# Kernel optimization log

Hardware: AMD Instinct MI355X
Metric: run time of the kernel (lower is better)

The kernel has to match this reference:

```python
import jax, jax.numpy as jnp
import numpy as np

MAX_ITER = 10
EPSILON = 1e-4


def setup_inputs() -> dict:
    key = jax.random.key(0)
    k1, k2 = jax.random.split(key)
    B, N1, N2 = 128, 512, 512
    s = jax.random.uniform(k1, (B, N1, N2), dtype=jnp.float32)
    # per-sample effective sizes; original module assumes nrows[b] == ncols[b]
    nrows = jax.random.randint(k2, (B,), 256, N1 + 1, dtype=jnp.int32)
    ncols = nrows
    return {"s": s, "nrows": nrows, "ncols": ncols}


def reference(s, nrows, ncols):
    """Faithful BiStochastic (masked Sinkhorn) forward.

    Even iter i: column-normalize within the [ncols, ncols] top-left block,
    zero everything outside the block (matches s * tmp with tmp zero outside).
    Odd  iter i: row-normalize within the [nrows, nrows] block, zero outside.
    """
    B, n1, n2 = s.shape
    i1 = jnp.arange(n1)
    i2 = jnp.arange(n2)
    # masks derived from the block-ones matrices in the original code
    cmask_r = i1[None, :] < ncols[:, None]           # [B, n1] rows < ncols
    cmask_c = i2[None, :] < ncols[:, None]           # [B, n2] cols < ncols
    rmask_r = i1[None, :] < nrows[:, None]           # [B, n1] rows < nrows
    rmask_c = i2[None, :] < nrows[:, None]           # [B, n2] cols < nrows
    col_block = cmask_r[:, :, None] & cmask_c[:, None, :]  # [B, n1, n2]
    row_block = rmask_r[:, :, None] & rmask_c[:, None, :]  # [B, n1, n2]

    s = s + EPSILON
    for i in range(MAX_ITER):
        if i % 2 == 0:
            # col_sum[b, c] = sum_{r < ncols[b]} s[b, r, c]
            col_sum = jnp.sum(jnp.where(cmask_r[:, :, None], s, 0.0),
                              axis=1, keepdims=True)          # [B, 1, n2]
            denom = jnp.where(col_block, col_sum, 1.0)
            s = jnp.where(col_block, s, 0.0) / denom
        else:
            # row_sum[b, r] = sum_{c < nrows[b]} s[b, r, c]
            row_sum = jnp.sum(jnp.where(rmask_c[:, None, :], s, 0.0),
                              axis=2, keepdims=True)          # [B, n1, 1]
            denom = jnp.where(row_block, row_sum, 1.0)
            s = jnp.where(row_block, s, 0.0) / denom
    return s
```

## Files before the change

### kernel.cpp

```cpp
#include <hip/hip_runtime.h>

#define N     512
#define NSP   4
#define SC    128
#define EPS   1e-4f

#define MROW  65
#define LDS_U   (512 * MROW + 512 + 128 * 33 + 128 + 64)
#define LDS_BYTES (LDS_U * 4)

union U32H { unsigned int u; _Float16 h[2]; };
__device__ inline float h_lo(unsigned int x){ U32H t; t.u = x; return (float)t.h[0]; }
__device__ inline float h_hi(unsigned int x){ U32H t; t.u = x; return (float)t.h[1]; }
__device__ inline unsigned int h_pk(float a, float b){ U32H t; t.h[0]=(_Float16)a; t.h[1]=(_Float16)b; return t.u; }

typedef _Float16 half2v __attribute__((ext_vector_type(2)));
#if __has_builtin(__builtin_amdgcn_fdot2)
__device__ inline float dot2(unsigned int m, unsigned int v, float c){
    return __builtin_amdgcn_fdot2(__builtin_bit_cast(half2v, m), __builtin_bit_cast(half2v, v), c, false);
}
#else
__device__ inline float dot2(unsigned int m, unsigned int v, float c){
    return c + h_lo(m)*h_lo(v) + h_hi(m)*h_hi(v);
}
#endif

typedef unsigned int uint4v __attribute__((ext_vector_type(4)));

__device__ inline void rp_store(float* p, float v){
    __hip_atomic_store(p, v, __ATOMIC_RELAXED, __HIP_MEMORY_SCOPE_AGENT);
}
__device__ inline float rp_load(float* p){
    return __hip_atomic_load(p, __ATOMIC_RELAXED, __HIP_MEMORY_SCOPE_AGENT);
}


#define SAMPLE_SYNC() do {                                                    \
    asm volatile("s_waitcnt vmcnt(0)" ::: "memory");                          \
    __syncthreads();                                                          \
    ++phase;                                                                  \
    if (t == 0) {                                                             \
        __hip_atomic_fetch_add(barb, 1u, __ATOMIC_RELAXED,                    \
                               __HIP_MEMORY_SCOPE_AGENT);                     \
        const unsigned int tgt_ = (unsigned int)(phase * NSP);                \
        while (__hip_atomic_fetch_add(barb, 0u, __ATOMIC_RELAXED,             \
                                      __HIP_MEMORY_SCOPE_AGENT) < tgt_) {     \
            __builtin_amdgcn_s_sleep(8);                                      \
        }                                                                     \
    }                                                                         \
    __syncthreads();                                                          \
} while (0)

#define COL_REDUCE() do {                                                     \
    _Pragma("unroll")                                                         \
    for (int k_ = 0; k_ < 8; ++k_) sh[(8*j + k_)*33 + part] = acc[k_];        \
    __syncthreads();                                                          \
    if (t < 128) {                                                            \
        float s_ = 0.f;                                                       \
        _Pragma("unroll")                                                     \
        for (int p_ = 0; p_ < 32; ++p_) s_ += sh[t*33 + p_];                  \
        vf[t] = (c0 + t < n) ? 1.f / s_ : 0.f;                                \
    }                                                                         \
    __syncthreads();                                                          \
    if (t < 64) vpk[t] = h_pk(vf[2*t], vf[2*t+1]);                            \
    __syncthreads();                                                          \
} while (0)

#define ROW_PART(RPOUT) do {                                                  \
    const unsigned int vp0_ = vpk[4*j+0], vp1_ = vpk[4*j+1];                  \
    const unsigned int vp2_ = vpk[4*j+2], vp3_ = vpk[4*j+3];                  \
    _Pragma("unroll")                                                         \
    for (int it_ = 0; it_ < 16; ++it_) {                                      \
        float p_ = dot2(m[it_][0], vp0_, 0.f);                                \
        p_ = dot2(m[it_][1], vp1_, p_);                                       \
        p_ = dot2(m[it_][2], vp2_, p_);                                       \
        p_ = dot2(m[it_][3], vp3_, p_);                                       \
        sh[(it_*32 + part)*17 + j] = p_;                                      \
    }                                                                         \
    __syncthreads();                                                          \
    {                                                                         \
        float s_ = 0.f;                                                       \
        _Pragma("unroll")                                                     \
        for (int q_ = 0; q_ < 16; ++q_) s_ += sh[t*17 + q_];                  \
        rp_store((RPOUT) + rpOff + t, s_);                                    \
    }                                                                         \
    __syncthreads();                                                          \
} while (0)

__global__ __launch_bounds__(512, 2)
void k_fused(const float* __restrict__ A, const int* __restrict__ nrows,
             float* __restrict__ rpA, float* __restrict__ rpB,
             float* __restrict__ out, unsigned int* __restrict__ bar) {
    __shared__ float sh[512*17];
    __shared__ float uu[512];
    __shared__ float vf[128];
    __shared__ unsigned int vpk[64];

    const int b = blockIdx.y, sp = blockIdx.x, c0 = sp * SC;
    const int n = nrows[b];
    const int t = threadIdx.x;
    const int l = t & 63;
    const int j = l & 15;
    const int part = (t >> 6) * 4 + (l >> 4);
    const size_t baseA = (size_t)b * N * N;
    const int cb = c0 + 8*j;
    const size_t rpOff = ((size_t)b * NSP + sp) * N;
    const size_t rpB0  = (size_t)b * NSP * N;
    unsigned int* barb = bar + (size_t)b * 32;
    int phase = 0;

    uint4v m[16];
    float acc[8];

    {
        bool cok0 = (cb+0) < n, cok1 = (cb+1) < n, cok2 = (cb+2) < n, cok3 = (cb+3) < n;
        bool cok4 = (cb+4) < n, cok5 = (cb+5) < n, cok6 = (cb+6) < n, cok7 = (cb+7) < n;
#pragma unroll
        for (int k = 0; k < 8; ++k) acc[k] = 0.f;
#pragma unroll
        for (int it = 0; it < 16; ++it) {
            const int r = it*32 + part;
            const float4* p = (const float4*)(A + baseA + (size_t)r*N + cb);
            float4 a0 = p[0], a1 = p[1];
            const bool rok = r < n;
            float e0 = (rok & cok0) ? a0.x + EPS : 0.f;
            float e1 = (rok & cok1) ? a0.y + EPS : 0.f;
            float e2 = (rok & cok2) ? a0.z + EPS : 0.f;
            float e3 = (rok & cok3) ? a0.w + EPS : 0.f;
            float e4 = (rok & cok4) ? a1.x + EPS : 0.f;
            float e5 = (rok & cok5) ? a1.y + EPS : 0.f;
            float e6 = (rok & cok6) ? a1.z + EPS : 0.f;
            float e7 = (rok & cok7) ? a1.w + EPS : 0.f;
            acc[0] += e0; acc[1] += e1; acc[2] += e2; acc[3] += e3;
            acc[4] += e4; acc[5] += e5; acc[6] += e6; acc[7] += e7;
            m[it][0] = h_pk(e0, e1);
            m[it][1] = h_pk(e2, e3);
            m[it][2] = h_pk(e4, e5);
            m[it][3] = h_pk(e6, e7);
        }
    }
    COL_REDUCE();
    ROW_PART(rpA);
    SAMPLE_SYNC();

    float* rIn = rpA; float* rOut = rpB;
    for (int ps = 0; ps < 4; ++ps) {
        {
            float s = rp_load(rIn + rpB0 + 0*N + t) + rp_load(rIn + rpB0 + 1*N + t)
                    + rp_load(rIn + rpB0 + 2*N + t) + rp_load(rIn + rpB0 + 3*N + t);
            uu[t] = (t < n) ? 1.f / s : 0.f;
        }
        __syncthreads();
#pragma unroll
        for (int k = 0; k < 8; ++k) acc[k] = 0.f;
#pragma unroll
        for (int it = 0; it < 16; ++it) {
            const float ur = uu[it*32 + part];
            acc[0] += ur * h_lo(m[it][0]);
            acc[1] += ur * h_hi(m[it][0]);
            acc[2] += ur * h_lo(m[it][1]);
            acc[3] += ur * h_hi(m[it][1]);
            acc[4] += ur * h_lo(m[it][2]);
            acc[5] += ur * h_hi(m[it][2]);
            acc[6] += ur * h_lo(m[it][3]);
            acc[7] += ur * h_hi(m[it][3]);
        }
        COL_REDUCE();
        ROW_PART(rOut);
        SAMPLE_SYNC();
        float* tmp = rIn; rIn = rOut; rOut = tmp;
    }

    {
        float s = rp_load(rIn + rpB0 + 0*N + t) + rp_load(rIn + rpB0 + 1*N + t)
                + rp_load(rIn + rpB0 + 2*N + t) + rp_load(rIn + rpB0 + 3*N + t);
        uu[t] = (t < n) ? 1.f / s : 0.f;
    }
    __syncthreads();
    const float v0 = vf[8*j+0], v1 = vf[8*j+1], v2 = vf[8*j+2], v3 = vf[8*j+3];
    const float v4 = vf[8*j+4], v5 = vf[8*j+5], v6 = vf[8*j+6], v7 = vf[8*j+7];
#pragma unroll
    for (int it = 0; it < 16; ++it) {
        const int r = it*32 + part;
        const float ur = uu[r];
        float4 o0, o1;
        o0.x = h_lo(m[it][0]) * ur * v0;
        o0.y = h_hi(m[it][0]) * ur * v1;
        o0.z = h_lo(m[it][1]) * ur * v2;
        o0.w = h_hi(m[it][1]) * ur * v3;
        o1.x = h_lo(m[it][2]) * ur * v4;
        o1.y = h_hi(m[it][2]) * ur * v5;
        o1.z = h_lo(m[it][3]) * ur * v6;
        o1.w = h_hi(m[it][3]) * ur * v7;
        float4* q = (float4*)(out + baseA + (size_t)r*N + cb);
        q[0] = o0; q[1] = o1;
    }
}


__device__ inline void pass_tail(unsigned int* M2, float* red, float* vf, unsigned int* vpk,
                                 const float acc[8], int t, int part, int j, int c0, int n,
                                 int b, int sp, float* __restrict__ rp_out,
                                 float* __restrict__ vf_out) {
#pragma unroll
    for (int k = 0; k < 8; ++k) red[(8*j + k)*33 + part] = acc[k];
    __syncthreads();
    if (t < 128) {
        float s = 0.f;
#pragma unroll
        for (int p = 0; p < 32; ++p) s += red[t*33 + p];
        float v = (c0 + t < n) ? 1.f / s : 0.f;
        vf[t] = v;
        if (vf_out) vf_out[b*N + c0 + t] = v;
    }
    __syncthreads();
    if (t < 64) vpk[t] = h_pk(vf[2*t], vf[2*t+1]);
    __syncthreads();
    float p = 0.f;
    const unsigned int* row = M2 + t * MROW;
#pragma unroll
    for (int q = 0; q < 64; ++q) p = dot2(row[q], vpk[q], p);
    rp_out[((size_t)b*NSP + sp)*N + t] = p;
}

__global__ __launch_bounds__(512)
void k_pass0(const float* __restrict__ A, const int* __restrict__ nrows,
             unsigned int* __restrict__ Abf, float* __restrict__ rp_out) {
    extern __shared__ unsigned int lds[];
    unsigned int* M2 = lds;
    float* uu = (float*)(lds + 512*MROW);
    float* red = uu + 512;
    float* vf  = red + 128*33;
    unsigned int* vpk = (unsigned int*)(vf + 128);

    const int b = blockIdx.y, sp = blockIdx.x, c0 = sp * SC;
    const int n = nrows[b];
    const int t = threadIdx.x;
    const int w = t >> 6, l = t & 63;
    const int j = l & 15, rg = l >> 4;
    const size_t baseA = (size_t)b * N * N;
    const size_t baseH = (size_t)b * N * (N/2);
    const int cb = c0 + 8*j;

    bool cok[8];
#pragma unroll
    for (int k = 0; k < 8; ++k) cok[k] = (cb + k) < n;

    float acc[8] = {0,0,0,0,0,0,0,0};
    for (int it = 0; it < 16; ++it) {
        int r = it*32 + w*4 + rg;
        const float4* p = (const float4*)(A + baseA + (size_t)r*N + cb);
        float4 a0 = p[0], a1 = p[1];
        bool rok = r < n;
        float e[8];
        e[0] = (rok && cok[0]) ? a0.x + EPS : 0.f;
        e[1] = (rok && cok[1]) ? a0.y + EPS : 0.f;
        e[2] = (rok && cok[2]) ? a0.z + EPS : 0.f;
        e[3] = (rok && cok[3]) ? a0.w + EPS : 0.f;
        e[4] = (rok && cok[4]) ? a1.x + EPS : 0.f;
        e[5] = (rok && cok[5]) ? a1.y + EPS : 0.f;
        e[6] = (rok && cok[6]) ? a1.z + EPS : 0.f;
        e[7] = (rok && cok[7]) ? a1.w + EPS : 0.f;
#pragma unroll
        for (int k = 0; k < 8; ++k) acc[k] += e[k];
        uint4 q;
        q.x = h_pk(e[0], e[1]); q.y = h_pk(e[2], e[3]);
        q.z = h_pk(e[4], e[5]); q.w = h_pk(e[6], e[7]);
        *(uint4*)(Abf + baseH + (size_t)r*(N/2) + c0/2 + 4*j) = q;
        unsigned int* dst = M2 + r*MROW + 4*j;
        dst[0] = q.x; dst[1] = q.y; dst[2] = q.z; dst[3] = q.w;
    }
    (void)uu;
    pass_tail(M2, red, vf, vpk, acc, t, w*4 + rg, j, c0, n, b, sp, rp_out, nullptr);
}

__global__ __launch_bounds__(512)
void k_passN(const unsigned int* __restrict__ Abf, const int* __restrict__ nrows,
             const float* __restrict__ rp_in, float* __restrict__ rp_out,
             float* __restrict__ vf_out) {
    extern __shared__ unsigned int lds[];
    unsigned int* M2 = lds;
    float* uu = (float*)(lds + 512*MROW);
    float* red = uu + 512;
    float* vf  = red + 128*33;
    unsigned int* vpk = (unsigned int*)(vf + 128);

    const int b = blockIdx.y, sp = blockIdx.x, c0 = sp * SC;
    const int n = nrows[b];
    const int t = threadIdx.x;
    const int w = t >> 6, l = t & 63;
    const int j = l & 15, rg = l >> 4;
    const size_t baseH = (size_t)b * N * (N/2);

    {
        float s = rp_in[((size_t)b*NSP + 0)*N + t]
                + rp_in[((size_t)b*NSP + 1)*N + t]
                + rp_in[((size_t)b*NSP + 2)*N + t]
                + rp_in[((size_t)b*NSP + 3)*N + t];
        uu[t] = (t < n) ? 1.f / s : 0.f;
    }
    __syncthreads();

    float acc[8] = {0,0,0,0,0,0,0,0};
    for (int it = 0; it < 16; ++it) {
        int r = it*32 + w*4 + rg;
        uint4 q = *(const uint4*)(Abf + baseH + (size_t)r*(N/2) + c0/2 + 4*j);
        float ur = uu[r];
        acc[0] += ur * h_lo(q.x); acc[1] += ur * h_hi(q.x);
        acc[2] += ur * h_lo(q.y); acc[3] += ur * h_hi(q.y);
        acc[4] += ur * h_lo(q.z); acc[5] += ur * h_hi(q.z);
        acc[6] += ur * h_lo(q.w); acc[7] += ur * h_hi(q.w);
        unsigned int* dst = M2 + r*MROW + 4*j;
        dst[0] = q.x; dst[1] = q.y; dst[2] = q.z; dst[3] = q.w;
    }
    __syncthreads();
    pass_tail(M2, red, vf, vpk, acc, t, w*4 + rg, j, c0, n, b, sp, rp_out, vf_out);
}

__global__ __launch_bounds__(512)
void k_epi(const float* __restrict__ A, const int* __restrict__ nrows,
           const float* __restrict__ rp9, const float* __restrict__ vf8,
           float* __restrict__ out) {
    const int b = blockIdx.y;
    const int n = nrows[b];
    const int t = threadIdx.x;
    const int r = blockIdx.x*4 + (t >> 7);
    const int c = (t & 127) * 4;
    float s = rp9[((size_t)b*NSP + 0)*N + r]
            + rp9[((size_t)b*NSP + 1)*N + r]
            + rp9[((size_t)b*NSP + 2)*N + r]
            + rp9[((size_t)b*NSP + 3)*N + r];
    float ur = (r < n) ? 1.f / s : 0.f;
    float4 v = *(const float4*)(vf8 + b*N + c);
    const size_t off = (size_t)b*N*N + (size_t)r*N + c;
    float4 a = *(const float4*)(A + off);
    float4 o;
    o.x = (a.x + EPS) * ur * v.x;
    o.y = (a.y + EPS) * ur * v.y;
    o.z = (a.z + EPS) * ur * v.z;
    o.w = (a.w + EPS) * ur * v.w;
    *(float4*)(out + off) = o;
}

extern "C" void kernel_launch(void* const* d_in, const int* in_sizes, int n_in,
                              void* d_out, int out_size, void* d_ws, size_t ws_size,
                              hipStream_t stream) {
    const float* A     = (const float*)d_in[0];
    const int*   nrows = (const int*)d_in[1];
    float*       out   = (float*)d_out;
    const int    B     = in_sizes[1];

    float* rpA = (float*)d_ws;
    float* rpB = rpA + (size_t)B * NSP * N;
    float* vf8 = rpB + (size_t)B * NSP * N;
    unsigned int* bar = (unsigned int*)((char*)d_ws + (4u << 20));

    do {
        if (hipMemsetAsync(bar, 0, (size_t)B * 32 * sizeof(unsigned int),
                           stream) != hipSuccess) break;
        void* args[] = { (void*)&A, (void*)&nrows, (void*)&rpA, (void*)&rpB,
                         (void*)&out, (void*)&bar };
        hipError_t err = hipLaunchCooperativeKernel(
            reinterpret_cast<const void*>(&k_fused),
            dim3(NSP, B), dim3(512), args, 0, stream);
        if (err == hipSuccess) return;
    } while (0);

    size_t head = ((size_t)2*B*NSP*N + (size_t)B*N) * sizeof(float);
    size_t abf_bytes = (size_t)B * N * (N/2) * sizeof(unsigned int);
    unsigned int* Abf = (ws_size >= head + abf_bytes)
                      ? (unsigned int*)((char*)d_ws + head)
                      : (unsigned int*)d_out;

    hipFuncSetAttribute(reinterpret_cast<const void*>(k_pass0),
                        hipFuncAttributeMaxDynamicSharedMemorySize, LDS_BYTES);
    hipFuncSetAttribute(reinterpret_cast<const void*>(k_passN),
                        hipFuncAttributeMaxDynamicSharedMemorySize, LDS_BYTES);

    dim3 g(NSP, B);
    k_pass0<<<g, 512, LDS_BYTES, stream>>>(A, nrows, Abf, rpA);
    k_passN<<<g, 512, LDS_BYTES, stream>>>(Abf, nrows, rpA, rpB, nullptr);
    k_passN<<<g, 512, LDS_BYTES, stream>>>(Abf, nrows, rpB, rpA, nullptr);
    k_passN<<<g, 512, LDS_BYTES, stream>>>(Abf, nrows, rpA, rpB, nullptr);
    k_passN<<<g, 512, LDS_BYTES, stream>>>(Abf, nrows, rpB, rpA, vf8);
    k_epi<<<dim3(N/4, B), 512, 0, stream>>>(A, nrows, rpA, vf8, out);
}
```

Baseline: 289.8 us.

## Launch fused kernel directly with XCD-aware block remap and shorter barrier sleep

Drops the cooperative-launch path and the multi-kernel fallback, and launches the fused per-sample kernel as a plain 1D grid. Block indices are remapped so the four column-split blocks of one sample have the same index modulo 8, which places them on the same XCD under round-robin dispatch and keeps the barrier atomics and row-partial exchanges in one L2. The spin-wait sleep is shortened to cut barrier wake-up latency. Without cooperative launch, co-residency of all blocks is no longer guaranteed, so the inter-block barrier could deadlock if the grid does not fit on the device at once.

```diff
diff --git a/kernel.cpp b/kernel.cpp
--- a/kernel.cpp
+++ b/kernel.cpp
@@ -4,10 +4,6 @@
 #define NSP   4
 #define SC    128
 #define EPS   1e-4f
-
-#define MROW  65
-#define LDS_U   (512 * MROW + 512 + 128 * 33 + 128 + 64)
-#define LDS_BYTES (LDS_U * 4)
 
 union U32H { unsigned int u; _Float16 h[2]; };
 __device__ inline float h_lo(unsigned int x){ U32H t; t.u = x; return (float)t.h[0]; }
@@ -45,7 +41,7 @@
         const unsigned int tgt_ = (unsigned int)(phase * NSP);                \
         while (__hip_atomic_fetch_add(barb, 0u, __ATOMIC_RELAXED,             \
                                       __HIP_MEMORY_SCOPE_AGENT) < tgt_) {     \
-            __builtin_amdgcn_s_sleep(8);                                      \
+            __builtin_amdgcn_s_sleep(2);                                      \
         }                                                                     \
     }                                                                         \
     __syncthreads();                                                          \
@@ -96,7 +92,12 @@
     __shared__ float vf[128];
     __shared__ unsigned int vpk[64];
 
-    const int b = blockIdx.y, sp = blockIdx.x, c0 = sp * SC;
+    const int g  = blockIdx.x;
+    const int c_ = g & 7;
+    const int q_ = g >> 3;
+    const int sp = q_ & 3;
+    const int b  = ((q_ >> 2) << 3) | c_;
+    const int c0 = sp * SC;
     const int n = nrows[b];
     const int t = threadIdx.x;
     const int l = t & 63;
@@ -197,151 +198,6 @@
     }
 }
 
-
-__device__ inline void pass_tail(unsigned int* M2, float* red, float* vf, unsigned int* vpk,
-                                 const float acc[8], int t, int part, int j, int c0, int n,
-                                 int b, int sp, float* __restrict__ rp_out,
-                                 float* __restrict__ vf_out) {
-#pragma unroll
-    for (int k = 0; k < 8; ++k) red[(8*j + k)*33 + part] = acc[k];
-    __syncthreads();
-    if (t < 128) {
-        float s = 0.f;
-#pragma unroll
-        for (int p = 0; p < 32; ++p) s += red[t*33 + p];
-        float v = (c0 + t < n) ? 1.f / s : 0.f;
-        vf[t] = v;
-        if (vf_out) vf_out[b*N + c0 + t] = v;
-    }
-    __syncthreads();
-    if (t < 64) vpk[t] = h_pk(vf[2*t], vf[2*t+1]);
-    __syncthreads();
-    float p = 0.f;
-    const unsigned int* row = M2 + t * MROW;
-#pragma unroll
-    for (int q = 0; q < 64; ++q) p = dot2(row[q], vpk[q], p);
-    rp_out[((size_t)b*NSP + sp)*N + t] = p;
-}
-
-__global__ __launch_bounds__(512)
-void k_pass0(const float* __restrict__ A, const int* __restrict__ nrows,
-             unsigned int* __restrict__ Abf, float* __restrict__ rp_out) {
-    extern __shared__ unsigned int lds[];
-    unsigned int* M2 = lds;
-    float* uu = (float*)(lds + 512*MROW);
-    float* red = uu + 512;
-    float* vf  = red + 128*33;
-    unsigned int* vpk = (unsigned int*)(vf + 128);
-
-    const int b = blockIdx.y, sp = blockIdx.x, c0 = sp * SC;
-    const int n = nrows[b];
-    const int t = threadIdx.x;
-    const int w = t >> 6, l = t & 63;
-    const int j = l & 15, rg = l >> 4;
-    const size_t baseA = (size_t)b * N * N;
-    const size_t baseH = (size_t)b * N * (N/2);
-    const int cb = c0 + 8*j;
-
-    bool cok[8];
-#pragma unroll
-    for (int k = 0; k < 8; ++k) cok[k] = (cb + k) < n;
-
-    float acc[8] = {0,0,0,0,0,0,0,0};
-    for (int it = 0; it < 16; ++it) {
-        int r = it*32 + w*4 + rg;
-        const float4* p = (const float4*)(A + baseA + (size_t)r*N + cb);
-        float4 a0 = p[0], a1 = p[1];
-        bool rok = r < n;
-        float e[8];
-        e[0] = (rok && cok[0]) ? a0.x + EPS : 0.f;
-        e[1] = (rok && cok[1]) ? a0.y + EPS : 0.f;
-        e[2] = (rok && cok[2]) ? a0.z + EPS : 0.f;
-        e[3] = (rok && cok[3]) ? a0.w + EPS : 0.f;
-        e[4] = (rok && cok[4]) ? a1.x + EPS : 0.f;
-        e[5] = (rok && cok[5]) ? a1.y + EPS : 0.f;
-        e[6] = (rok && cok[6]) ? a1.z + EPS : 0.f;
-        e[7] = (rok && cok[7]) ? a1.w + EPS : 0.f;
-#pragma unroll
-        for (int k = 0; k < 8; ++k) acc[k] += e[k];
-        uint4 q;
-        q.x = h_pk(e[0], e[1]); q.y = h_pk(e[2], e[3]);
-        q.z = h_pk(e[4], e[5]); q.w = h_pk(e[6], e[7]);
-        *(uint4*)(Abf + baseH + (size_t)r*(N/2) + c0/2 + 4*j) = q;
-        unsigned int* dst = M2 + r*MROW + 4*j;
-        dst[0] = q.x; dst[1] = q.y; dst[2] = q.z; dst[3] = q.w;
-    }
-    (void)uu;
-    pass_tail(M2, red, vf, vpk, acc, t, w*4 + rg, j, c0, n, b, sp, rp_out, nullptr);
-}
-
-__global__ __launch_bounds__(512)
-void k_passN(const unsigned int* __restrict__ Abf, const int* __restrict__ nrows,
-             const float* __restrict__ rp_in, float* __restrict__ rp_out,
-             float* __restrict__ vf_out) {
-    extern __shared__ unsigned int lds[];
-    unsigned int* M2 = lds;
-    float* uu = (float*)(lds + 512*MROW);
-    float* red = uu + 512;
-    float* vf  = red + 128*33;
-    unsigned int* vpk = (unsigned int*)(vf + 128);
-
-    const int b = blockIdx.y, sp = blockIdx.x, c0 = sp * SC;
-    const int n = nrows[b];
-    const int t = threadIdx.x;
-    const int w = t >> 6, l = t & 63;
-    const int j = l & 15, rg = l >> 4;
-    const size_t baseH = (size_t)b * N * (N/2);
-
-    {
-        float s = rp_in[((size_t)b*NSP + 0)*N + t]
-                + rp_in[((size_t)b*NSP + 1)*N + t]
-                + rp_in[((size_t)b*NSP + 2)*N + t]
-                + rp_in[((size_t)b*NSP + 3)*N + t];
-        uu[t] = (t < n) ? 1.f / s : 0.f;
-    }
-    __syncthreads();
-
-    float acc[8] = {0,0,0,0,0,0,0,0};
-    for (int it = 0; it < 16; ++it) {
-        int r = it*32 + w*4 + rg;
-        uint4 q = *(const uint4*)(Abf + baseH + (size_t)r*(N/2) + c0/2 + 4*j);
-        float ur = uu[r];
-        acc[0] += ur * h_lo(q.x); acc[1] += ur * h_hi(q.x);
-        acc[2] += ur * h_lo(q.y); acc[3] += ur * h_hi(q.y);
-        acc[4] += ur * h_lo(q.z); acc[5] += ur * h_hi(q.z);
-        acc[6] += ur * h_lo(q.w); acc[7] += ur * h_hi(q.w);
-        unsigned int* dst = M2 + r*MROW + 4*j;
-        dst[0] = q.x; dst[1] = q.y; dst[2] = q.z; dst[3] = q.w;
-    }
-    __syncthreads();
-    pass_tail(M2, red, vf, vpk, acc, t, w*4 + rg, j, c0, n, b, sp, rp_out, vf_out);
-}
-
-__global__ __launch_bounds__(512)
-void k_epi(const float* __restrict__ A, const int* __restrict__ nrows,
-           const float* __restrict__ rp9, const float* __restrict__ vf8,
-           float* __restrict__ out) {
-    const int b = blockIdx.y;
-    const int n = nrows[b];
-    const int t = threadIdx.x;
-    const int r = blockIdx.x*4 + (t >> 7);
-    const int c = (t & 127) * 4;
-    float s = rp9[((size_t)b*NSP + 0)*N + r]
-            + rp9[((size_t)b*NSP + 1)*N + r]
-            + rp9[((size_t)b*NSP + 2)*N + r]
-            + rp9[((size_t)b*NSP + 3)*N + r];
-    float ur = (r < n) ? 1.f / s : 0.f;
-    float4 v = *(const float4*)(vf8 + b*N + c);
-    const size_t off = (size_t)b*N*N + (size_t)r*N + c;
-    float4 a = *(const float4*)(A + off);
-    float4 o;
-    o.x = (a.x + EPS) * ur * v.x;
-    o.y = (a.y + EPS) * ur * v.y;
-    o.z = (a.z + EPS) * ur * v.z;
-    o.w = (a.w + EPS) * ur * v.w;
-    *(float4*)(out + off) = o;
-}
-
 extern "C" void kernel_launch(void* const* d_in, const int* in_sizes, int n_in,
                               void* d_out, int out_size, void* d_ws, size_t ws_size,
                               hipStream_t stream) {
@@ -352,36 +208,8 @@
 
     float* rpA = (float*)d_ws;
     float* rpB = rpA + (size_t)B * NSP * N;
-    float* vf8 = rpB + (size_t)B * NSP * N;
     unsigned int* bar = (unsigned int*)((char*)d_ws + (4u << 20));
 
-    do {
-        if (hipMemsetAsync(bar, 0, (size_t)B * 32 * sizeof(unsigned int),
-                           stream) != hipSuccess) break;
-        void* args[] = { (void*)&A, (void*)&nrows, (void*)&rpA, (void*)&rpB,
-                         (void*)&out, (void*)&bar };
-        hipError_t err = hipLaunchCooperativeKernel(
-            reinterpret_cast<const void*>(&k_fused),
-            dim3(NSP, B), dim3(512), args, 0, stream);
-        if (err == hipSuccess) return;
-    } while (0);
-
-    size_t head = ((size_t)2*B*NSP*N + (size_t)B*N) * sizeof(float);
-    size_t abf_bytes = (size_t)B * N * (N/2) * sizeof(unsigned int);
-    unsigned int* Abf = (ws_size >= head + abf_bytes)
-                      ? (unsigned int*)((char*)d_ws + head)
-                      : (unsigned int*)d_out;
-
-    hipFuncSetAttribute(reinterpret_cast<const void*>(k_pass0),
-                        hipFuncAttributeMaxDynamicSharedMemorySize, LDS_BYTES);
-    hipFuncSetAttribute(reinterpret_cast<const void*>(k_passN),
-                        hipFuncAttributeMaxDynamicSharedMemorySize, LDS_BYTES);
-
-    dim3 g(NSP, B);
-    k_pass0<<<g, 512, LDS_BYTES, stream>>>(A, nrows, Abf, rpA);
-    k_passN<<<g, 512, LDS_BYTES, stream>>>(Abf, nrows, rpA, rpB, nullptr);
-    k_passN<<<g, 512, LDS_BYTES, stream>>>(Abf, nrows, rpB, rpA, nullptr);
-    k_passN<<<g, 512, LDS_BYTES, stream>>>(Abf, nrows, rpA, rpB, nullptr);
-    k_passN<<<g, 512, LDS_BYTES, stream>>>(Abf, nrows, rpB, rpA, vf8);
-    k_epi<<<dim3(N/4, B), 512, 0, stream>>>(A, nrows, rpA, vf8, out);
-}
+    hipMemsetAsync(bar, 0, (size_t)B * 32 * sizeof(unsigned int), stream);
+    k_fused<<<dim3(NSP * B), dim3(512), 0, stream>>>(A, nrows, rpA, rpB, out, bar);
+}
```

Measured after the change: 269.0 us. 1.08x faster.
